# Kernel optimization log

Measured on AMD Instinct MI355X. Metric: run time of the kernel, lower is better.

The kernel has to match this reference:

```python
import jax, jax.numpy as jnp
import numpy as np
from jax import lax

N_NODES = 150_000
N_EDGES = 1_500_000
N_GRAPHS = 150          # batch_size(30) * sequence_length(5), hardcoded in forward
BATCH_SIZE = 30
SEQ_LEN = 5
IN_F = 1
HID = 100               # gcn_hidden_size == lstm_hidden_size


def setup_inputs() -> dict:
    key = jax.random.key(0)
    ks = jax.random.split(key, 12)
    x = jax.random.normal(ks[0], (N_NODES, IN_F), dtype=jnp.float32)
    edge_index = jax.random.randint(ks[1], (2, N_EDGES), 0, N_NODES, dtype=jnp.int32)
    # 150 graphs of 1000 nodes each (contiguous, as PyG batching produces)
    batch = jnp.repeat(jnp.arange(N_GRAPHS, dtype=jnp.int32), N_NODES // N_GRAPHS)
    s = 0.1
    params = {
        # GCNConv layer 1: Linear(no bias) weight stored [in, out]; separate bias
        "W1": jax.random.normal(ks[2], (IN_F, HID), jnp.float32) * s,
        "b1": jnp.zeros((HID,), jnp.float32),
        # GCNConv layer 2
        "W2": jax.random.normal(ks[3], (HID, HID), jnp.float32) * s,
        "b2": jnp.zeros((HID,), jnp.float32),
        # LSTM (PyTorch gate order i,f,g,o), weights [4H, in]/[4H, H]
        "W_ih": jax.random.normal(ks[4], (4 * HID, HID), jnp.float32) * s,
        "W_hh": jax.random.normal(ks[5], (4 * HID, HID), jnp.float32) * s,
        "b_ih": jnp.zeros((4 * HID,), jnp.float32),
        "b_hh": jnp.zeros((4 * HID,), jnp.float32),
        # output head Linear(HID, 1)
        "W_out": jax.random.normal(ks[6], (1, HID), jnp.float32) * s,
        "b_out": jnp.zeros((1,), jnp.float32),
    }
    return {"x": x, "edge_index": edge_index, "batch": batch, **params}


def _gcn_conv(x, src, dst, W, b, n_nodes):
    """PyG GCNConv: h = W x; out = D^-1/2 (A+I) D^-1/2 h + b."""
    h = x @ W  # [N, HID]
    deg = jax.ops.segment_sum(jnp.ones_like(dst, dtype=h.dtype), dst, num_segments=n_nodes)
    dinv = lax.rsqrt(deg)  # deg >= 1 thanks to self loops
    norm = dinv[src] * dinv[dst]  # [E+N]
    msg = h[src] * norm[:, None]  # gather + scale (memory-bound hot loop)
    out = jax.ops.segment_sum(msg, dst, num_segments=n_nodes)
    return out + b


def _lstm_last_hidden(xs, W_ih, W_hh, b_ih, b_hh):
    """xs: [B, T, H] -> last hidden state [B, H] (single-layer LSTM)."""
    B = xs.shape[0]
    H = W_hh.shape[1]
    h0 = jnp.zeros((B, H), xs.dtype)
    c0 = jnp.zeros((B, H), xs.dtype)

    def step(carry, xt):
        h, c = carry
        gates = xt @ W_ih.T + h @ W_hh.T + (b_ih + b_hh)
        i, f, g, o = jnp.split(gates, 4, axis=-1)
        c = jax.nn.sigmoid(f) * c + jax.nn.sigmoid(i) * jnp.tanh(g)
        h = jax.nn.sigmoid(o) * jnp.tanh(c)
        return (h, c), None

    (h_last, _), _ = lax.scan(step, (h0, c0), jnp.swapaxes(xs, 0, 1))
    return h_last


def reference(x, edge_index, batch, W1, b1, W2, b2, W_ih, W_hh, b_ih, b_hh, W_out, b_out):
    n_nodes = x.shape[0]
    loops = jnp.arange(n_nodes, dtype=edge_index.dtype)
    src = jnp.concatenate([edge_index[0], loops])
    dst = jnp.concatenate([edge_index[1], loops])

    h = _gcn_conv(x, src, dst, W1, b1, n_nodes)
    h = _gcn_conv(h, src, dst, W2, b2, n_nodes)

    # global mean pool over 150 graphs
    sums = jax.ops.segment_sum(h, batch, num_segments=N_GRAPHS)
    cnts = jax.ops.segment_sum(jnp.ones((n_nodes,), h.dtype), batch, num_segments=N_GRAPHS)
    pooled = sums / jnp.maximum(cnts, 1.0)[:, None]  # [150, HID]

    seq = pooled.reshape(BATCH_SIZE, SEQ_LEN, -1)  # [30, 5, HID]
    h_last = _lstm_last_hidden(seq, W_ih, W_hh, b_ih, b_hh)
    prediction = h_last @ W_out.T + b_out  # [30, 1]
    return prediction
```

## Files before the change

### kernel.cpp

```cpp
#include <hip/hip_runtime.h>
#include <math.h>

#define N_NODES   150000
#define N_EDGES   1500000
#define N_GRAPHS  150
#define HID       100
#define BATCH     30
#define SEQ       5
#define NODES_PER_GRAPH 1000

#define NPB   512
#define NB    293
#define SBLK  128
#define SORT_T 512
#define ACC_T 512
#define NREP  4
#define EPB   11720
#define CAP   5632
#define DLMASK 511

__global__ __launch_bounds__(SORT_T) void k_s1(const int* __restrict__ dst,
                                               int* __restrict__ blockBase) {
    __shared__ int hist[NB];
    int t = threadIdx.x;
    for (int i = t; i < NB; i += SORT_T) hist[i] = 0;
    __syncthreads();
    int base = blockIdx.x * EPB;
    int end  = min(base + EPB, N_EDGES);
    for (int i = base + t * 4; i < end; i += SORT_T * 4) {
        int4 d = *reinterpret_cast<const int4*>(dst + i);
        atomicAdd(&hist[d.x >> 9], 1);
        atomicAdd(&hist[d.y >> 9], 1);
        atomicAdd(&hist[d.z >> 9], 1);
        atomicAdd(&hist[d.w >> 9], 1);
    }
    __syncthreads();
    for (int j = t; j < NB; j += SORT_T)
        blockBase[blockIdx.x * NB + j] = hist[j];
}

__global__ __launch_bounds__(SBLK) void k_colscan(int* __restrict__ blockBase,
                                                  int* __restrict__ bucketCount) {
    __shared__ int v[SBLK];
    int j = blockIdx.x;
    int t = threadIdx.x;
    int val = blockBase[t * NB + j];
    v[t] = val;
    __syncthreads();
    for (int off = 1; off < SBLK; off <<= 1) {
        int w = (t >= off) ? v[t - off] : 0;
        __syncthreads();
        v[t] += w;
        __syncthreads();
    }
    blockBase[t * NB + j] = v[t] - val;
    if (t == SBLK - 1) bucketCount[j] = v[t];
}

__global__ __launch_bounds__(SORT_T) void k_s2(const int* __restrict__ src,
                                               const int* __restrict__ dst,
                                               const int* __restrict__ blockBase,
                                               unsigned int* __restrict__ sorted) {
    __shared__ int cursor[NB];
    __shared__ int baseS[NB];
    int t = threadIdx.x;
    const int* bb = blockBase + blockIdx.x * NB;
    for (int i = t; i < NB; i += SORT_T) {
        cursor[i] = 0;
        baseS[i] = i * CAP + bb[i];
    }
    __syncthreads();
    int base = blockIdx.x * EPB;
    int end  = min(base + EPB, N_EDGES);
    for (int i = base + t * 4; i < end; i += SORT_T * 4) {
        int4 s4 = *reinterpret_cast<const int4*>(src + i);
        int4 d4 = *reinterpret_cast<const int4*>(dst + i);
        int bk[4] = { d4.x >> 9, d4.y >> 9, d4.z >> 9, d4.w >> 9 };
        int sv[4] = { s4.x, s4.y, s4.z, s4.w };
        int dl[4] = { d4.x & DLMASK, d4.y & DLMASK, d4.z & DLMASK, d4.w & DLMASK };
        #pragma unroll
        for (int k = 0; k < 4; ++k) {
            int b = bk[k];
            int idx = atomicAdd(&cursor[b], 1);
            sorted[baseS[b] + idx] = ((unsigned int)sv[k] << 9) | (unsigned int)dl[k];
        }
    }
}

__device__ __forceinline__ void bin2_reduce_store(float2 acc, float2* red2, int t,
                                                  float2* __restrict__ outp) {
    red2[t] = acc;
    __syncthreads();
    for (int s = ACC_T / 2; s > 0; s >>= 1) {
        if (t < s) { red2[t].x += red2[t + s].x; red2[t].y += red2[t + s].y; }
        __syncthreads();
    }
    if (t == 0) *outp = red2[0];
}

__global__ __launch_bounds__(ACC_T) void k_accA(const unsigned int* __restrict__ sorted,
                                                const int* __restrict__ bucketCount,
                                                const float* __restrict__ x,
                                                float* __restrict__ pd,
                                                float* __restrict__ px,
                                                float2* __restrict__ pW) {
    __shared__ int degI[NREP][NPB];
    __shared__ float2 red2[ACC_T];
    int b = blockIdx.x;
    int t = threadIdx.x;
    int n0 = b << 9;
    int nn = min(NPB, N_NODES - n0);
    #pragma unroll
    for (int r = 0; r < NREP; ++r) degI[r][t] = 0;
    __syncthreads();
    int e0 = b * CAP, e1 = e0 + bucketCount[b];
    int rep = t & (NREP - 1);
    int nvec = (e1 - e0) >> 2;
    for (int v = t; v < nvec; v += ACC_T) {
        uint4 u4 = *reinterpret_cast<const uint4*>(sorted + e0 + v * 4);
        atomicAdd(&degI[rep][u4.x & DLMASK], 1);
        atomicAdd(&degI[rep][u4.y & DLMASK], 1);
        atomicAdd(&degI[rep][u4.z & DLMASK], 1);
        atomicAdd(&degI[rep][u4.w & DLMASK], 1);
    }
    int tail0 = e0 + (nvec << 2);
    if (tail0 + t < e1) atomicAdd(&degI[rep][sorted[tail0 + t] & DLMASK], 1);
    __syncthreads();
    int g0 = n0 / 1000;
    int thresh = (g0 + 1) * 1000 - n0;
    float2 acc = make_float2(0.f, 0.f);
    if (t < nn) {
        int dsum = 1 + degI[0][t] + degI[1][t] + degI[2][t] + degI[3][t];
        float dv = 1.0f / sqrtf((float)dsum);
        pd[n0 + t] = dv;
        px[n0 + t] = dv * x[n0 + t];
        float v = dv * dv;
        if (t < thresh) acc.x += v; else acc.y += v;
    }
    bin2_reduce_store(acc, red2, t, &pW[b]);
}

__global__ __launch_bounds__(ACC_T) void k_accB(const unsigned int* __restrict__ sorted,
                                                const int* __restrict__ bucketCount,
                                                const float* __restrict__ pd,
                                                const float* __restrict__ px,
                                                float2* __restrict__ pa2,
                                                float2* __restrict__ pA) {
    __shared__ float t1s[NREP][NPB];
    __shared__ float2 red2[ACC_T];
    int b = blockIdx.x;
    int t = threadIdx.x;
    int n0 = b << 9;
    int nn = min(NPB, N_NODES - n0);
    #pragma unroll
    for (int r = 0; r < NREP; ++r) t1s[r][t] = 0.0f;
    __syncthreads();
    int e0 = b * CAP, e1 = e0 + bucketCount[b];
    int rep = t & (NREP - 1);
    int nvec = (e1 - e0) >> 2;
    for (int v = t; v < nvec; v += ACC_T) {
        uint4 u4 = *reinterpret_cast<const uint4*>(sorted + e0 + v * 4);
        float p0 = px[u4.x >> 9];
        float p1 = px[u4.y >> 9];
        float p2 = px[u4.z >> 9];
        float p3 = px[u4.w >> 9];
        atomicAdd(&t1s[rep][u4.x & DLMASK], p0);
        atomicAdd(&t1s[rep][u4.y & DLMASK], p1);
        atomicAdd(&t1s[rep][u4.z & DLMASK], p2);
        atomicAdd(&t1s[rep][u4.w & DLMASK], p3);
    }
    int tail0 = e0 + (nvec << 2);
    if (tail0 + t < e1) {
        unsigned int u = sorted[tail0 + t];
        atomicAdd(&t1s[rep][u & DLMASK], px[u >> 9]);
    }
    __syncthreads();
    int g0 = n0 / 1000;
    int thresh = (g0 + 1) * 1000 - n0;
    float2 acc = make_float2(0.f, 0.f);
    if (t < nn) {
        float dv = pd[n0 + t];
        float T1 = t1s[0][t] + t1s[1][t] + t1s[2][t] + t1s[3][t];
        float agg1 = dv * T1 + dv * px[n0 + t];
        float a1 = dv * agg1;
        pa2[n0 + t] = make_float2(dv, a1);
        float v = dv * a1;
        if (t < thresh) acc.x += v; else acc.y += v;
    }
    bin2_reduce_store(acc, red2, t, &pA[b]);
}

__global__ __launch_bounds__(ACC_T) void k_accG(const unsigned int* __restrict__ sorted,
                                                const int* __restrict__ bucketCount,
                                                const float2* __restrict__ pa2,
                                                float4* __restrict__ pG) {
    __shared__ float dvl[NPB];
    __shared__ float4 red4[ACC_T];
    int b = blockIdx.x;
    int t = threadIdx.x;
    int n0 = b << 9;
    int nn = min(NPB, N_NODES - n0);
    dvl[t] = (t < nn) ? pa2[n0 + t].x : 0.0f;
    __syncthreads();
    int g0 = n0 / 1000;
    int thresh = (g0 + 1) * 1000 - n0;
    float sa0 = 0.f, sa1 = 0.f, sw0 = 0.f, sw1 = 0.f;
    int e0 = b * CAP, e1 = e0 + bucketCount[b];
    auto proc = [&](unsigned int u) {
        int dl = (int)(u & DLMASK);
        float dvd = dvl[dl];
        float2 v = pa2[u >> 9];
        if (dl < thresh) { sw0 += dvd * v.x; sa0 += dvd * v.y; }
        else             { sw1 += dvd * v.x; sa1 += dvd * v.y; }
    };
    int nvec = (e1 - e0) >> 2;
    for (int v = t; v < nvec; v += ACC_T) {
        uint4 u4 = *reinterpret_cast<const uint4*>(sorted + e0 + v * 4);
        proc(u4.x); proc(u4.y); proc(u4.z); proc(u4.w);
    }
    int tail0 = e0 + (nvec << 2);
    if (tail0 + t < e1) proc(sorted[tail0 + t]);
    red4[t] = make_float4(sa0, sa1, sw0, sw1);
    __syncthreads();
    for (int s = ACC_T / 2; s > 0; s >>= 1) {
        if (t < s) {
            red4[t].x += red4[t + s].x; red4[t].y += red4[t + s].y;
            red4[t].z += red4[t + s].z; red4[t].w += red4[t + s].w;
        }
        __syncthreads();
    }
    if (t == 0) pG[b] = red4[0];
}

__global__ __launch_bounds__(512) void k_tail(const float2* __restrict__ pW,
                                              const float2* __restrict__ pA,
                                              const float4* __restrict__ pG,
                                              const float* __restrict__ W1,
                                              const float* __restrict__ b1,
                                              const float* __restrict__ W2,
                                              const float* __restrict__ b2,
                                              const float* __restrict__ W_ih,
                                              const float* __restrict__ W_hh,
                                              const float* __restrict__ b_ih,
                                              const float* __restrict__ b_hh,
                                              const float* __restrict__ W_out,
                                              const float* __restrict__ b_out,
                                              float* __restrict__ outp) {
    int b = blockIdx.x;
    int t = threadIdx.x;
    __shared__ float gA[N_GRAPHS], gW[N_GRAPHS];
    __shared__ float v1[HID], v2[HID];
    __shared__ float xs_l[SEQ][HID];
    __shared__ float Xg_l[SEQ][4 * HID];
    __shared__ float hs[HID], cs[HID], gsb[4 * HID];
    __shared__ float red[512];

    if (t < N_GRAPHS) { gA[t] = 0.0f; gW[t] = 0.0f; }
    __syncthreads();
    for (int j = t; j < NB; j += 512) {
        int n0 = j << 9;
        int g0 = n0 / 1000;
        float2 w2v = pW[j];
        float2 a2v = pA[j];
        float4 g4 = pG[j];
        atomicAdd(&gA[g0], a2v.x + g4.x);
        atomicAdd(&gW[g0], w2v.x + g4.z);
        if (g0 + 1 < N_GRAPHS) {
            atomicAdd(&gA[g0 + 1], a2v.y + g4.y);
            atomicAdd(&gW[g0 + 1], w2v.y + g4.w);
        }
    }
    if (t < HID) {
        float a = 0.0f, c = 0.0f;
        for (int k = 0; k < HID; ++k) {
            float w2 = W2[k * HID + t];
            a += W1[k] * w2;
            c += b1[k] * w2;
        }
        v1[t] = a; v2[t] = c;
    }
    __syncthreads();

    if (t < SEQ * HID) {
        int s = t / HID, j = t - s * HID;
        int g = b * SEQ + s;
        float ma = gA[g] * (1.0f / NODES_PER_GRAPH);
        float mw = gW[g] * (1.0f / NODES_PER_GRAPH);
        xs_l[s][j] = ma * v1[j] + mw * v2[j] + b2[j];
    }
    __syncthreads();

    float wreg[HID];
    if (t < 4 * HID) {
        const float4* wp = reinterpret_cast<const float4*>(W_ih + t * HID);
        #pragma unroll
        for (int q = 0; q < HID / 4; ++q) {
            float4 w4 = wp[q];
            wreg[4*q+0] = w4.x; wreg[4*q+1] = w4.y; wreg[4*q+2] = w4.z; wreg[4*q+3] = w4.w;
        }
        float bias = b_ih[t] + b_hh[t];
        for (int s = 0; s < SEQ; ++s) {
            float acc = bias;
            #pragma unroll
            for (int k = 0; k < HID; ++k)
                acc += xs_l[s][k] * wreg[k];
            Xg_l[s][t] = acc;
        }
        wp = reinterpret_cast<const float4*>(W_hh + t * HID);
        #pragma unroll
        for (int q = 0; q < HID / 4; ++q) {
            float4 w4 = wp[q];
            wreg[4*q+0] = w4.x; wreg[4*q+1] = w4.y; wreg[4*q+2] = w4.z; wreg[4*q+3] = w4.w;
        }
    }
    if (t < HID) { hs[t] = 0.0f; cs[t] = 0.0f; }
    __syncthreads();

    for (int step = 0; step < SEQ; ++step) {
        if (t < 4 * HID) {
            float acc = Xg_l[step][t];
            #pragma unroll
            for (int k = 0; k < HID; ++k)
                acc += hs[k] * wreg[k];
            gsb[t] = acc;
        }
        __syncthreads();
        if (t < HID) {
            float ig = 1.0f / (1.0f + expf(-gsb[t]));
            float fg = 1.0f / (1.0f + expf(-gsb[HID + t]));
            float gg = tanhf(gsb[2 * HID + t]);
            float og = 1.0f / (1.0f + expf(-gsb[3 * HID + t]));
            float c  = fg * cs[t] + ig * gg;
            cs[t] = c;
            hs[t] = og * tanhf(c);
        }
        __syncthreads();
    }

    float v = (t < HID) ? hs[t] * W_out[t] : 0.0f;
    red[t] = v;
    __syncthreads();
    for (int s = 256; s > 0; s >>= 1) {
        if (t < s) red[t] += red[t + s];
        __syncthreads();
    }
    if (t == 0) outp[b] = red[0] + b_out[0];
}

static inline char* align_up(char* p, size_t a) {
    return (char*)(((uintptr_t)p + (a - 1)) & ~(uintptr_t)(a - 1));
}

extern "C" void kernel_launch(void* const* d_in, const int* in_sizes, int n_in,
                              void* d_out, int out_size, void* d_ws, size_t ws_size,
                              hipStream_t stream) {
    const float* x    = (const float*)d_in[0];
    const int*   ei   = (const int*)d_in[1];
    const int*   srcp = ei;
    const int*   dstp = ei + N_EDGES;
    const float* W1   = (const float*)d_in[3];
    const float* b1   = (const float*)d_in[4];
    const float* W2   = (const float*)d_in[5];
    const float* b2   = (const float*)d_in[6];
    const float* W_ih = (const float*)d_in[7];
    const float* W_hh = (const float*)d_in[8];
    const float* b_ih = (const float*)d_in[9];
    const float* b_hh = (const float*)d_in[10];
    const float* W_out= (const float*)d_in[11];
    const float* b_out= (const float*)d_in[12];
    float* out = (float*)d_out;

    char* w = (char*)d_ws;
    int*  bucketCount = (int*)w;             w = align_up(w + NB * sizeof(int), 64);
    int*  blockBase   = (int*)w;             w = align_up(w + (size_t)SBLK * NB * sizeof(int), 64);
    unsigned int* sorted = (unsigned int*)w; w = align_up(w + (size_t)NB * CAP * sizeof(unsigned int), 64);
    float*  pd  = (float*)w;                 w = align_up(w + (size_t)N_NODES * sizeof(float), 64);
    float*  px  = (float*)w;                 w = align_up(w + (size_t)N_NODES * sizeof(float), 64);
    float2* pa2 = (float2*)w;                w = align_up(w + (size_t)N_NODES * sizeof(float2), 64);
    float2* pW  = (float2*)w;                w = align_up(w + NB * sizeof(float2), 64);
    float2* pA  = (float2*)w;                w = align_up(w + NB * sizeof(float2), 64);
    float4* pG  = (float4*)w;                w = align_up(w + NB * sizeof(float4), 64);

    k_s1     <<<SBLK, SORT_T, 0, stream>>>(dstp, blockBase);
    k_colscan<<<NB, SBLK, 0, stream>>>(blockBase, bucketCount);
    k_s2     <<<SBLK, SORT_T, 0, stream>>>(srcp, dstp, blockBase, sorted);
    k_accA   <<<NB, ACC_T, 0, stream>>>(sorted, bucketCount, x, pd, px, pW);
    k_accB   <<<NB, ACC_T, 0, stream>>>(sorted, bucketCount, pd, px, pa2, pA);
    k_accG   <<<NB, ACC_T, 0, stream>>>(sorted, bucketCount, pa2, pG);
    k_tail   <<<BATCH, 512, 0, stream>>>(pW, pA, pG, W1, b1, W2, b2,
                                         W_ih, W_hh, b_ih, b_hh, W_out, b_out, out);
}
```

Before: 81.02 us.

## Fuse bucket sort into single kernel using LDS staging and global atomic offsets

```diff
diff --git a/kernel.cpp b/kernel.cpp
--- a/kernel.cpp
+++ b/kernel.cpp
@@ -11,79 +11,54 @@
 
 #define NPB   512
 #define NB    293
-#define SBLK  128
+#define SBLK  256
 #define SORT_T 512
 #define ACC_T 512
 #define NREP  4
-#define EPB   11720
+#define EPB   5860
 #define CAP   5632
 #define DLMASK 511
 
-__global__ __launch_bounds__(SORT_T) void k_s1(const int* __restrict__ dst,
-                                               int* __restrict__ blockBase) {
+__global__ __launch_bounds__(SORT_T) void k_sort(const int* __restrict__ src,
+                                                 const int* __restrict__ dst,
+                                                 int* __restrict__ bucketCount,
+                                                 unsigned int* __restrict__ sorted) {
+    __shared__ unsigned int   epack[EPB];
+    __shared__ unsigned short ebuck[EPB];
     __shared__ int hist[NB];
+    __shared__ int baseS[NB];
     int t = threadIdx.x;
     for (int i = t; i < NB; i += SORT_T) hist[i] = 0;
-    __syncthreads();
-    int base = blockIdx.x * EPB;
-    int end  = min(base + EPB, N_EDGES);
-    for (int i = base + t * 4; i < end; i += SORT_T * 4) {
-        int4 d = *reinterpret_cast<const int4*>(dst + i);
-        atomicAdd(&hist[d.x >> 9], 1);
-        atomicAdd(&hist[d.y >> 9], 1);
-        atomicAdd(&hist[d.z >> 9], 1);
-        atomicAdd(&hist[d.w >> 9], 1);
-    }
-    __syncthreads();
-    for (int j = t; j < NB; j += SORT_T)
-        blockBase[blockIdx.x * NB + j] = hist[j];
-}
-
-__global__ __launch_bounds__(SBLK) void k_colscan(int* __restrict__ blockBase,
-                                                  int* __restrict__ bucketCount) {
-    __shared__ int v[SBLK];
-    int j = blockIdx.x;
-    int t = threadIdx.x;
-    int val = blockBase[t * NB + j];
-    v[t] = val;
-    __syncthreads();
-    for (int off = 1; off < SBLK; off <<= 1) {
-        int w = (t >= off) ? v[t - off] : 0;
-        __syncthreads();
-        v[t] += w;
-        __syncthreads();
-    }
-    blockBase[t * NB + j] = v[t] - val;
-    if (t == SBLK - 1) bucketCount[j] = v[t];
-}
-
-__global__ __launch_bounds__(SORT_T) void k_s2(const int* __restrict__ src,
-                                               const int* __restrict__ dst,
-                                               const int* __restrict__ blockBase,
-                                               unsigned int* __restrict__ sorted) {
-    __shared__ int cursor[NB];
-    __shared__ int baseS[NB];
-    int t = threadIdx.x;
-    const int* bb = blockBase + blockIdx.x * NB;
-    for (int i = t; i < NB; i += SORT_T) {
-        cursor[i] = 0;
-        baseS[i] = i * CAP + bb[i];
-    }
     __syncthreads();
     int base = blockIdx.x * EPB;
     int end  = min(base + EPB, N_EDGES);
     for (int i = base + t * 4; i < end; i += SORT_T * 4) {
         int4 s4 = *reinterpret_cast<const int4*>(src + i);
         int4 d4 = *reinterpret_cast<const int4*>(dst + i);
-        int bk[4] = { d4.x >> 9, d4.y >> 9, d4.z >> 9, d4.w >> 9 };
+        int l = i - base;
         int sv[4] = { s4.x, s4.y, s4.z, s4.w };
         int dl[4] = { d4.x & DLMASK, d4.y & DLMASK, d4.z & DLMASK, d4.w & DLMASK };
+        int bk[4] = { d4.x >> 9, d4.y >> 9, d4.z >> 9, d4.w >> 9 };
         #pragma unroll
         for (int k = 0; k < 4; ++k) {
-            int b = bk[k];
-            int idx = atomicAdd(&cursor[b], 1);
-            sorted[baseS[b] + idx] = ((unsigned int)sv[k] << 9) | (unsigned int)dl[k];
-        }
+            atomicAdd(&hist[bk[k]], 1);
+            epack[l + k] = ((unsigned int)sv[k] << 9) | (unsigned int)dl[k];
+            ebuck[l + k] = (unsigned short)bk[k];
+        }
+    }
+    __syncthreads();
+    for (int j = t; j < NB; j += SORT_T) {
+        int c = hist[j];
+        int gb = (c > 0) ? atomicAdd(&bucketCount[j], c) : 0;
+        baseS[j] = j * CAP + gb;
+        hist[j] = 0;
+    }
+    __syncthreads();
+    int nloc = end - base;
+    for (int l = t; l < nloc; l += SORT_T) {
+        int bk = ebuck[l];
+        int idx = atomicAdd(&hist[bk], 1);
+        sorted[baseS[bk] + idx] = epack[l];
     }
 }
 
@@ -372,7 +347,6 @@
 
     char* w = (char*)d_ws;
     int*  bucketCount = (int*)w;             w = align_up(w + NB * sizeof(int), 64);
-    int*  blockBase   = (int*)w;             w = align_up(w + (size_t)SBLK * NB * sizeof(int), 64);
     unsigned int* sorted = (unsigned int*)w; w = align_up(w + (size_t)NB * CAP * sizeof(unsigned int), 64);
     float*  pd  = (float*)w;                 w = align_up(w + (size_t)N_NODES * sizeof(float), 64);
     float*  px  = (float*)w;                 w = align_up(w + (size_t)N_NODES * sizeof(float), 64);
@@ -381,12 +355,11 @@
     float2* pA  = (float2*)w;                w = align_up(w + NB * sizeof(float2), 64);
     float4* pG  = (float4*)w;                w = align_up(w + NB * sizeof(float4), 64);
 
-    k_s1     <<<SBLK, SORT_T, 0, stream>>>(dstp, blockBase);
-    k_colscan<<<NB, SBLK, 0, stream>>>(blockBase, bucketCount);
-    k_s2     <<<SBLK, SORT_T, 0, stream>>>(srcp, dstp, blockBase, sorted);
-    k_accA   <<<NB, ACC_T, 0, stream>>>(sorted, bucketCount, x, pd, px, pW);
-    k_accB   <<<NB, ACC_T, 0, stream>>>(sorted, bucketCount, pd, px, pa2, pA);
-    k_accG   <<<NB, ACC_T, 0, stream>>>(sorted, bucketCount, pa2, pG);
-    k_tail   <<<BATCH, 512, 0, stream>>>(pW, pA, pG, W1, b1, W2, b2,
-                                         W_ih, W_hh, b_ih, b_hh, W_out, b_out, out);
-}
+    hipMemsetAsync(bucketCount, 0, NB * sizeof(int), stream);
+    k_sort<<<SBLK, SORT_T, 0, stream>>>(srcp, dstp, bucketCount, sorted);
+    k_accA<<<NB, ACC_T, 0, stream>>>(sorted, bucketCount, x, pd, px, pW);
+    k_accB<<<NB, ACC_T, 0, stream>>>(sorted, bucketCount, pd, px, pa2, pA);
+    k_accG<<<NB, ACC_T, 0, stream>>>(sorted, bucketCount, pa2, pG);
+    k_tail<<<BATCH, 512, 0, stream>>>(pW, pA, pG, W1, b1, W2, b2,
+                                      W_ih, W_hh, b_ih, b_hh, W_out, b_out, out);
+}
```

Measured after the change: 82.30 us. Within noise of the previous version (+1.6%).
